# Kernel tuning notes

Measured on AMD Instinct MI355X. Metric: run time of the kernel, lower is better.

Reference implementation:

```python
import jax, jax.numpy as jnp
import numpy as np

B, C, H, W, E = 32, 64, 64, 64, 8

def setup_inputs() -> dict:
    key = jax.random.key(0)
    k1, k2, k3 = jax.random.split(key, 3)
    x = jax.random.normal(k1, (B, C, H, W), dtype=jnp.float32)
    gate_w = jax.random.normal(k2, (E, C, 3, 3), dtype=jnp.float32) * 0.02
    gate_b = jnp.zeros((E,), dtype=jnp.float32)
    expert_w = jax.random.normal(k3, (E, C, C), dtype=jnp.float32) * 0.05  # per-expert 1x1 conv (out,in)
    return {"x": x, "gate_w": gate_w, "gate_b": gate_b, "expert_w": expert_w}

def reference(x, gate_w, gate_b, expert_w):
    # Gating: Conv2d(C->E, k=3, stride=1, VALID), then sum over both spatial dims -> [B, E]
    g = jax.lax.conv_general_dilated(
        x, gate_w, window_strides=(1, 1), padding='VALID',
        dimension_numbers=('NCHW', 'OIHW', 'NCHW'))
    g = g + gate_b[None, :, None, None]
    gating_code = jnp.sum(g, axis=(2, 3))                      # [B, E]
    # softmax over experts then top-1
    probs = jax.nn.softmax(gating_code, axis=1)                # [B, E]
    top1_val = jnp.max(probs, axis=1)                          # [B]
    top1_idx = jnp.argmax(probs, axis=1)                       # [B]
    onehot = jax.nn.one_hot(top1_idx, E, dtype=x.dtype)        # [B, E]
    expert_weights = top1_val[:, None] * onehot                # combine tensor squeezed, [B, E]
    dispatch = onehot                                          # bool(combine) cast back to float == one-hot
    # einsum 'bjkd,ben->ebjkd' with n=1: broadcast x to every expert slot, masked by dispatch
    expert_inputs = x[None] * dispatch.T[:, :, None, None, None]   # [E, B, C, H, W]
    # experts: per-expert bias-free 1x1 conv (C -> C)
    expert_out = jnp.einsum('ebchw,efc->ebfhw', expert_inputs, expert_w)  # [E, B, C, H, W]
    # combine: einsum 'ij, ji... -> i...'
    output = jnp.einsum('be,ebchw->bchw', expert_weights, expert_out)      # [B, C, H, W]
    return output, expert_weights
```

## Files before the change

kernel.cpp:

```cpp
#include <hip/hip_runtime.h>

typedef float f4 __attribute__((ext_vector_type(4)));

#define BB 32
#define CC 64
#define EE 8
#define HWX 4096
#define PXT 128

__device__ __forceinline__ unsigned bf16r(float f) {
  unsigned u = __builtin_bit_cast(unsigned, f);
  u += 0x7FFFu + ((u >> 16) & 1u);
  return u >> 16;
}
__device__ __forceinline__ unsigned pack2(float a, float b) {
  return bf16r(a) | (bf16r(b) << 16);
}
__device__ __forceinline__ float ubf_lo(unsigned u) {
  return __builtin_bit_cast(float, u << 16);
}
__device__ __forceinline__ float ubf_hi(unsigned u) {
  return __builtin_bit_cast(float, u & 0xFFFF0000u);
}

__global__ __launch_bounds__(256) void k_gate_sums(
    const float* __restrict__ x, const float* __restrict__ gate_w,
    float* __restrict__ gpart) {
  __shared__ float sg[9];
  __shared__ float cor[4][4];
  __shared__ float sS[9];
  int t = threadIdx.x;
  int bc = blockIdx.x;
  int c = bc & 63;
  const float* plane = x + (size_t)bc * HWX;
  int h = t >> 2, q = t & 3;
  const f4* rp = (const f4*)(plane + h * 64 + q * 16);
  f4 a0 = rp[0], a1 = rp[1], a2 = rp[2], a3 = rp[3];
  float local = (a0[0]+a0[1]+a0[2]+a0[3]) + (a1[0]+a1[1]+a1[2]+a1[3])
              + (a2[0]+a2[1]+a2[2]+a2[3]) + (a3[0]+a3[1]+a3[2]+a3[3]);
  if (t < 9) sg[t] = 0.f;
  __syncthreads();

  bool special = (h < 2) || (h >= 62);
  int ridx = (h < 2) ? h : h - 60;

  float red = local;
  #pragma unroll
  for (int off = 32; off > 0; off >>= 1) red += __shfl_down(red, off, 64);
  if ((t & 63) == 0) atomicAdd(&sg[0], red);

  if (special) atomicAdd(&sg[1 + ridx], local);
  if (q == 0) {
    atomicAdd(&sg[5], a0[0]); atomicAdd(&sg[6], a0[1]);
    if (special) { cor[ridx][0] = a0[0]; cor[ridx][1] = a0[1]; }
  }
  if (q == 3) {
    atomicAdd(&sg[7], a3[2]); atomicAdd(&sg[8], a3[3]);
    if (special) { cor[ridx][2] = a3[2]; cor[ridx][3] = a3[3]; }
  }
  __syncthreads();

  if (t == 0) {
    const int EX[3][2] = {{2,3},{0,3},{0,1}};
    float T = sg[0];
    #pragma unroll
    for (int i = 0; i < 3; i++)
      #pragma unroll
      for (int j = 0; j < 3; j++) {
        float Re = sg[1 + EX[i][0]] + sg[1 + EX[i][1]];
        float Ce = sg[5 + EX[j][0]] + sg[5 + EX[j][1]];
        float Xc = cor[EX[i][0]][EX[j][0]] + cor[EX[i][0]][EX[j][1]]
                 + cor[EX[i][1]][EX[j][0]] + cor[EX[i][1]][EX[j][1]];
        sS[i * 3 + j] = T - Re - Ce + Xc;
      }
  }
  __syncthreads();

  if (t < EE) {
    const float* gw = gate_w + ((size_t)t * CC + c) * 9;
    float ge = 0.f;
    #pragma unroll
    for (int k = 0; k < 9; k++) ge += gw[k] * sS[k];
    int b = bc >> 6;
    gpart[b * (EE * CC) + t * CC + c] = ge;
  }
}

__global__ __launch_bounds__(256) void k_mix(
    const float* __restrict__ x, const float* __restrict__ expert_w,
    const float* __restrict__ gpart, const float* __restrict__ gate_b,
    float* __restrict__ out, float* __restrict__ ew_out) {
  __shared__ uint2 W2[64 * 16];
  __shared__ uint2 X2[64 * 32];
  __shared__ float gsh[EE];
  int t = threadIdx.x;
  int pt = blockIdx.x;
  int b  = blockIdx.y;

  const float* Xg = x + (size_t)b * CC * HWX + pt * PXT;
  #pragma unroll
  for (int k = 0; k < 8; k++) {
    int idx = t + 256 * k;
    int r = idx >> 5, q = idx & 31;
    f4 v = *(const f4*)(Xg + (size_t)r * HWX + (q << 2));
    uint2 p; p.x = pack2(v[0], v[1]); p.y = pack2(v[2], v[3]);
    X2[r * 32 + q] = p;
  }

  {
    int e = t >> 5, j = t & 31;
    const float* gp = gpart + b * (EE * CC) + e * CC;
    float gval = gp[j] + gp[j + 32];
    #pragma unroll
    for (int off = 16; off > 0; off >>= 1) gval += __shfl_down(gval, off, 32);
    if (j == 0) gsh[e] = gval + 3844.0f * gate_b[e];
  }
  __syncthreads();

  float g[EE];
  #pragma unroll
  for (int e = 0; e < EE; e++) g[e] = gsh[e];
  int best = 0; float bg = g[0];
  #pragma unroll
  for (int e = 1; e < EE; e++) if (g[e] > bg) { bg = g[e]; best = e; }
  float s = 0.f;
  #pragma unroll
  for (int e = 0; e < EE; e++) s += __expf(g[e] - bg);
  float sc = 1.0f / s;
  if (pt == 0 && t < EE) ew_out[b * EE + t] = (t == best) ? sc : 0.f;

  const float* Wg = expert_w + (size_t)best * (CC * CC);
  #pragma unroll
  for (int k = 0; k < 4; k++) {
    int idx = t + 256 * k;
    int r = idx >> 4, q = idx & 15;
    f4 v = *(const f4*)(Wg + r * CC + (q << 2));
    uint2 p; p.x = pack2(v[0], v[1]); p.y = pack2(v[2], v[3]);
    W2[r * 16 + q] = p;
  }
  __syncthreads();

  int f0 = (t >> 5) << 3;
  int px = t & 31;
  float acc[8][4] = {};
  #pragma unroll
  for (int cq = 0; cq < 16; cq++) {
    uint2 xu[4];
    #pragma unroll
    for (int j = 0; j < 4; j++) xu[j] = X2[((cq << 2) + j) * 32 + px];
    uint2 wu[8];
    #pragma unroll
    for (int i = 0; i < 8; i++) wu[i] = W2[(f0 + i) * 16 + cq];
    #pragma unroll
    for (int j = 0; j < 4; j++) {
      unsigned xr0 = xu[j].x, xr1 = xu[j].y;
      float xp0 = ubf_lo(xr0), xp1 = ubf_hi(xr0);
      float xp2 = ubf_lo(xr1), xp3 = ubf_hi(xr1);
      #pragma unroll
      for (int i = 0; i < 8; i++) {
        unsigned wraw = (j < 2) ? wu[i].x : wu[i].y;
        float wf = ((j & 1) == 0) ? ubf_lo(wraw) : ubf_hi(wraw);
        acc[i][0] += wf * xp0; acc[i][1] += wf * xp1;
        acc[i][2] += wf * xp2; acc[i][3] += wf * xp3;
      }
    }
  }

  float* Og = out + ((size_t)(b * CC + f0)) * HWX + pt * PXT + (px << 2);
  #pragma unroll
  for (int i = 0; i < 8; i++) {
    f4 r;
    r[0] = sc * acc[i][0]; r[1] = sc * acc[i][1];
    r[2] = sc * acc[i][2]; r[3] = sc * acc[i][3];
    *(f4*)(Og + (size_t)i * HWX) = r;
  }
}

extern "C" void kernel_launch(void* const* d_in, const int* in_sizes, int n_in,
                              void* d_out, int out_size, void* d_ws, size_t ws_size,
                              hipStream_t stream) {
  const float* x        = (const float*)d_in[0];
  const float* gate_w   = (const float*)d_in[1];
  const float* gate_b   = (const float*)d_in[2];
  const float* expert_w = (const float*)d_in[3];
  float* out = (float*)d_out;
  float* ew_out = out + (size_t)BB * CC * HWX;

  float* gpart = (float*)d_ws;

  k_gate_sums<<<BB * CC, 256, 0, stream>>>(x, gate_w, gpart);
  k_mix<<<dim3(HWX / PXT, BB), 256, 0, stream>>>(x, expert_w, gpart, gate_b,
                                                 out, ew_out);
}
```

Measured before the change: 110.8 us.

## Use bf16 MFMA for expert 1x1 conv instead of scalar FMA via LDS

Replaces the LDS-staged scalar FMA matmul in the mix kernel with MFMA 16x16x32 bf16 instructions. Weight fragments and x fragments are loaded directly from global memory into registers, dropping both shared-memory tiles and one barrier. The cost is scalar 4-byte global loads of x (16 lanes contiguous) and scalar output stores, which are less vectorised than the previous f4 accesses. Since the kernel is likely memory-bound, the gain depends on whether those narrower accesses hurt bandwidth.

Measured after the change: 102.8 us. 1.08x faster.

```diff
diff --git a/kernel.cpp b/kernel.cpp
--- a/kernel.cpp
+++ b/kernel.cpp
@@ -1,6 +1,8 @@
 #include <hip/hip_runtime.h>
 
 typedef float f4 __attribute__((ext_vector_type(4)));
+typedef short bf16x8 __attribute__((ext_vector_type(8)));
+typedef float f32x4 __attribute__((ext_vector_type(4)));
 
 #define BB 32
 #define CC 64
@@ -16,12 +18,8 @@
 __device__ __forceinline__ unsigned pack2(float a, float b) {
   return bf16r(a) | (bf16r(b) << 16);
 }
-__device__ __forceinline__ float ubf_lo(unsigned u) {
-  return __builtin_bit_cast(float, u << 16);
-}
-__device__ __forceinline__ float ubf_hi(unsigned u) {
-  return __builtin_bit_cast(float, u & 0xFFFF0000u);
-}
+
+union frag_cast { bf16x8 v; unsigned u[4]; };
 
 __global__ __launch_bounds__(256) void k_gate_sums(
     const float* __restrict__ x, const float* __restrict__ gate_w,
@@ -90,22 +88,10 @@
     const float* __restrict__ x, const float* __restrict__ expert_w,
     const float* __restrict__ gpart, const float* __restrict__ gate_b,
     float* __restrict__ out, float* __restrict__ ew_out) {
-  __shared__ uint2 W2[64 * 16];
-  __shared__ uint2 X2[64 * 32];
   __shared__ float gsh[EE];
   int t = threadIdx.x;
   int pt = blockIdx.x;
   int b  = blockIdx.y;
-
-  const float* Xg = x + (size_t)b * CC * HWX + pt * PXT;
-  #pragma unroll
-  for (int k = 0; k < 8; k++) {
-    int idx = t + 256 * k;
-    int r = idx >> 5, q = idx & 31;
-    f4 v = *(const f4*)(Xg + (size_t)r * HWX + (q << 2));
-    uint2 p; p.x = pack2(v[0], v[1]); p.y = pack2(v[2], v[3]);
-    X2[r * 32 + q] = p;
-  }
 
   {
     int e = t >> 5, j = t & 31;
@@ -129,50 +115,64 @@
   float sc = 1.0f / s;
   if (pt == 0 && t < EE) ew_out[b * EE + t] = (t == best) ? sc : 0.f;
 
+  int wave = t >> 6;
+  int lane = t & 63;
+  int l15  = lane & 15;
+  int quad = lane >> 4;
+
   const float* Wg = expert_w + (size_t)best * (CC * CC);
+  bf16x8 afr[4][2];
   #pragma unroll
-  for (int k = 0; k < 4; k++) {
-    int idx = t + 256 * k;
-    int r = idx >> 4, q = idx & 15;
-    f4 v = *(const f4*)(Wg + r * CC + (q << 2));
-    uint2 p; p.x = pack2(v[0], v[1]); p.y = pack2(v[2], v[3]);
-    W2[r * 16 + q] = p;
-  }
-  __syncthreads();
-
-  int f0 = (t >> 5) << 3;
-  int px = t & 31;
-  float acc[8][4] = {};
-  #pragma unroll
-  for (int cq = 0; cq < 16; cq++) {
-    uint2 xu[4];
+  for (int ft = 0; ft < 4; ft++) {
+    const float* wrow = Wg + (ft * 16 + l15) * CC + quad * 8;
     #pragma unroll
-    for (int j = 0; j < 4; j++) xu[j] = X2[((cq << 2) + j) * 32 + px];
-    uint2 wu[8];
-    #pragma unroll
-    for (int i = 0; i < 8; i++) wu[i] = W2[(f0 + i) * 16 + cq];
-    #pragma unroll
-    for (int j = 0; j < 4; j++) {
-      unsigned xr0 = xu[j].x, xr1 = xu[j].y;
-      float xp0 = ubf_lo(xr0), xp1 = ubf_hi(xr0);
-      float xp2 = ubf_lo(xr1), xp3 = ubf_hi(xr1);
-      #pragma unroll
-      for (int i = 0; i < 8; i++) {
-        unsigned wraw = (j < 2) ? wu[i].x : wu[i].y;
-        float wf = ((j & 1) == 0) ? ubf_lo(wraw) : ubf_hi(wraw);
-        acc[i][0] += wf * xp0; acc[i][1] += wf * xp1;
-        acc[i][2] += wf * xp2; acc[i][3] += wf * xp3;
-      }
+    for (int kk = 0; kk < 2; kk++) {
+      f4 w0 = *(const f4*)(wrow + kk * 32);
+      f4 w1 = *(const f4*)(wrow + kk * 32 + 4);
+      frag_cast fc;
+      fc.u[0] = pack2(w0[0], w0[1]); fc.u[1] = pack2(w0[2], w0[3]);
+      fc.u[2] = pack2(w1[0], w1[1]); fc.u[3] = pack2(w1[2], w1[3]);
+      afr[ft][kk] = fc.v;
     }
   }
 
-  float* Og = out + ((size_t)(b * CC + f0)) * HWX + pt * PXT + (px << 2);
+  const float* Xb = x + (size_t)b * CC * HWX + pt * PXT + 32 * wave;
+  f32x4 acc[2][4] = {};
   #pragma unroll
-  for (int i = 0; i < 8; i++) {
-    f4 r;
-    r[0] = sc * acc[i][0]; r[1] = sc * acc[i][1];
-    r[2] = sc * acc[i][2]; r[3] = sc * acc[i][3];
-    *(f4*)(Og + (size_t)i * HWX) = r;
+  for (int ss = 0; ss < 2; ss++) {
+    const float* xp = Xb + ss * 16 + l15 + (size_t)(quad * 8) * HWX;
+    #pragma unroll
+    for (int kk = 0; kk < 2; kk++) {
+      const float* xq = xp + (size_t)(kk * 32) * HWX;
+      float e0 = xq[0];
+      float e1 = xq[HWX];
+      float e2 = xq[2 * HWX];
+      float e3 = xq[3 * HWX];
+      float e4 = xq[4 * HWX];
+      float e5 = xq[5 * HWX];
+      float e6 = xq[6 * HWX];
+      float e7 = xq[7 * HWX];
+      frag_cast fb;
+      fb.u[0] = pack2(e0, e1); fb.u[1] = pack2(e2, e3);
+      fb.u[2] = pack2(e4, e5); fb.u[3] = pack2(e6, e7);
+      #pragma unroll
+      for (int ft = 0; ft < 4; ft++)
+        acc[ss][ft] = __builtin_amdgcn_mfma_f32_16x16x32_bf16(
+            afr[ft][kk], fb.v, acc[ss][ft], 0, 0, 0);
+    }
+  }
+
+  #pragma unroll
+  for (int ss = 0; ss < 2; ss++) {
+    #pragma unroll
+    for (int ft = 0; ft < 4; ft++) {
+      int f = ft * 16 + quad * 4;
+      float* Og = out + ((size_t)(b * CC + f)) * HWX
+                + pt * PXT + 32 * wave + ss * 16 + l15;
+      #pragma unroll
+      for (int r = 0; r < 4; r++)
+        Og[(size_t)r * HWX] = sc * acc[ss][ft][r];
+    }
   }
 }
 
```
